# Kernel optimization log

Measured on AMD Instinct MI355X. Metric: run time of the kernel, lower is better.

The kernel has to match this reference:

```python
import jax, jax.numpy as jnp
import numpy as np

B, S, H, I, E, TOPK = 2, 2048, 1024, 2048, 8, 2


def setup_inputs() -> dict:
    key = jax.random.key(0)
    ks = jax.random.split(key, 6)
    return {
        "x": jax.random.normal(ks[0], (B, S, H), dtype=jnp.float32),
        "expert_indices": jax.random.randint(ks[1], (B, S, TOPK), 0, E, dtype=jnp.int64),
        "expert_weights": jax.random.uniform(ks[2], (B, S, TOPK), dtype=jnp.float32),
        "gate_proj": jax.random.normal(ks[3], (E, I, H), dtype=jnp.float32) * 0.02,
        "up_proj": jax.random.normal(ks[4], (E, I, H), dtype=jnp.float32) * 0.02,
        "down_proj": jax.random.normal(ks[5], (E, H, I), dtype=jnp.float32) * 0.02,
    }


def reference(x, expert_indices, expert_weights, gate_proj, up_proj, down_proj):
    # x: [B,S,H]; expert_indices/weights: [B,S,K]; gate/up: [E,I,H]; down: [E,H,I]
    b, s, h = x.shape
    e = gate_proj.shape[0]
    xf = x.reshape(-1, h)                      # [T,H]
    t = xf.shape[0]
    idx = expert_indices.reshape(t, -1)        # [T,K]
    w = expert_weights.reshape(t, -1)          # [T,K]
    # Combine per-(token,slot) weights into a per-(token,expert) weight matrix.
    # Identical math to the per-expert index_add_ in the torch module.
    we = jnp.zeros((t, e), dtype=x.dtype).at[jnp.arange(t)[:, None], idx].add(w)  # [T,E]
    gate = jax.nn.silu(jnp.einsum('th,eih->tei', xf, gate_proj))  # [T,E,I]
    up = jnp.einsum('th,eih->tei', xf, up_proj)                   # [T,E,I]
    out_e = jnp.einsum('tei,ehi->teh', gate * up, down_proj)      # [T,E,H]
    out = jnp.einsum('te,teh->th', we, out_e)                     # [T,H]
    return out.reshape(b, s, h)
```

## Files before the change

kernel.cpp:

```cpp
#include <hip/hip_runtime.h>


#define H_DIM 1024
#define I_DIM 2048
#define N_EXP 8
#define N_TOK 4096
#define N_ENT 8192
#define CAP   9216

typedef __attribute__((ext_vector_type(8))) short bhalf8;
typedef __attribute__((ext_vector_type(4))) float floatx4;

__device__ __forceinline__ unsigned short f2bf(float f) {
  unsigned int u = __float_as_uint(f);
  u += 0x7fffu + ((u >> 16) & 1u);
  return (unsigned short)(u >> 16);
}

__device__ __forceinline__ void ld16(const void* g, void* l) {
  __builtin_amdgcn_global_load_lds(
      (const __attribute__((address_space(1))) unsigned int*)g,
      (__attribute__((address_space(3))) unsigned int*)l, 16, 0, 0);
}

__global__ __launch_bounds__(256) void route_kernel(
    const int* __restrict__ idx, const float* __restrict__ wts,
    int* __restrict__ perm, float* __restrict__ pw, int* __restrict__ inv,
    int* __restrict__ counts, int* __restrict__ poff)
{
  __shared__ int cnt[N_EXP], cur[N_EXP], off[N_EXP];
  const int t = threadIdx.x;
  if (t < N_EXP) { cnt[t] = 0; cur[t] = 0; }
  __syncthreads();
  for (int i = t; i < N_ENT; i += 256) atomicAdd(&cnt[idx[i] & 7], 1);
  __syncthreads();
  if (t == 0) {
    int o = 0;
    for (int e = 0; e < N_EXP; e++) {
      off[e] = o; counts[e] = cnt[e]; poff[e] = o;
      o += ((cnt[e] + 127) >> 7) << 7;
    }
  }
  __syncthreads();
  for (int i = t; i < N_ENT; i += 256) {
    int e = idx[i] & 7;
    int p = atomicAdd(&cur[e], 1);
    int pos = off[e] + p;
    perm[pos] = i >> 1;
    pw[pos] = wts[i];
    inv[i] = pos;
  }
}

#define XE  4194304u
#define GE  20971520u
#define UE  37748736u
#define DE  54525952u
__global__ __launch_bounds__(256) void cast_all_kernel(
    const float* __restrict__ x, const float* __restrict__ g4,
    const float* __restrict__ u4, const float* __restrict__ d4,
    unsigned short* __restrict__ dst)
{
  unsigned int g = (blockIdx.x * 256u + threadIdx.x) * 8u;
  const float* s;
  if (g < XE)      s = x  + g;
  else if (g < GE) s = g4 + (g - XE);
  else if (g < UE) s = u4 + (g - GE);
  else             s = d4 + (g - UE);
  const float4* sp = (const float4*)s;
  float4 a = sp[0], b = sp[1];
  bhalf8 o;
  o[0] = (short)f2bf(a.x); o[1] = (short)f2bf(a.y); o[2] = (short)f2bf(a.z); o[3] = (short)f2bf(a.w);
  o[4] = (short)f2bf(b.x); o[5] = (short)f2bf(b.y); o[6] = (short)f2bf(b.z); o[7] = (short)f2bf(b.w);
  *(bhalf8*)(dst + g) = o;
}

__global__ __launch_bounds__(512, 4) void gemm1_kernel(
    const unsigned short* __restrict__ xb,
    const unsigned short* __restrict__ gbw,
    const unsigned short* __restrict__ ubw,
    const int* __restrict__ perm,
    const int* __restrict__ counts,
    const int* __restrict__ poff,
    unsigned short* __restrict__ act)
{
  const int e = blockIdx.z;
  const int Ne = counts[e];
  const int mt = blockIdx.y;
  if (mt * 256 >= Ne) return;
  const int NeR = ((Ne + 127) >> 7) << 7;
  const int base = poff[e];
  const int n0 = blockIdx.x * 64;

  __shared__ __align__(16) unsigned short As[256 * 64];
  __shared__ __align__(16) unsigned short Bgs[64 * 64];
  __shared__ __align__(16) unsigned short Bus[64 * 64];

  const int tid = threadIdx.x;
  const int lane = tid & 63;
  const int w = tid >> 6;
  const int wmi = w >> 1;
  const int wnj = w & 1;
  const int i3 = lane >> 3, i7 = lane & 7;
  const int swc = (i7 ^ i3) * 8;

  const unsigned short* pA[4]; unsigned short* lA[4];
#pragma unroll
  for (int t = 0; t < 4; t++) {
    int rloc = w * 32 + t * 8 + i3;
    int rr = mt * 256 + rloc; rr = rr < Ne ? rr : Ne - 1;
    pA[t] = xb + (size_t)perm[base + rr] * H_DIM + swc;
    lA[t] = &As[(w * 32 + t * 8) * 64];
  }
  const int nloc = w * 8 + i3;
  const size_t wb = (size_t)e * (I_DIM * H_DIM) + (size_t)(n0 + nloc) * H_DIM + swc;
  const unsigned short* pBg = gbw + wb;
  const unsigned short* pBu = ubw + wb;
  unsigned short* lBg = &Bgs[(w * 8) * 64];
  unsigned short* lBu = &Bus[(w * 8) * 64];

  floatx4 zero = {0.f, 0.f, 0.f, 0.f};
  floatx4 accg[4][2], accu[4][2];
#pragma unroll
  for (int i = 0; i < 4; i++)
#pragma unroll
    for (int j = 0; j < 2; j++) { accg[i][j] = zero; accu[i][j] = zero; }

  const int quad = lane >> 4, lm = lane & 15;
  const int s7 = lm & 7;

  for (int k0 = 0; k0 < H_DIM; k0 += 64) {
    __syncthreads();
#pragma unroll
    for (int t = 0; t < 4; t++) ld16(pA[t] + k0, lA[t]);
    ld16(pBg + k0, lBg);
    ld16(pBu + k0, lBu);
    __syncthreads();
#pragma unroll
    for (int kk = 0; kk < 2; kk++) {
      const int kq = kk * 4 + quad;
      const int ko = (kq ^ s7) * 8;
      bhalf8 a[4], bg[2], bu[2];
#pragma unroll
      for (int i = 0; i < 4; i++)
        a[i] = *(const bhalf8*)&As[(wmi * 64 + i * 16 + lm) * 64 + ko];
#pragma unroll
      for (int j = 0; j < 2; j++) {
        bg[j] = *(const bhalf8*)&Bgs[(wnj * 32 + j * 16 + lm) * 64 + ko];
        bu[j] = *(const bhalf8*)&Bus[(wnj * 32 + j * 16 + lm) * 64 + ko];
      }
#pragma unroll
      for (int i = 0; i < 4; i++)
#pragma unroll
        for (int j = 0; j < 2; j++) {
          accg[i][j] = __builtin_amdgcn_mfma_f32_16x16x32_bf16(a[i], bg[j], accg[i][j], 0, 0, 0);
          accu[i][j] = __builtin_amdgcn_mfma_f32_16x16x32_bf16(a[i], bu[j], accu[i][j], 0, 0, 0);
        }
    }
  }

#pragma unroll
  for (int i = 0; i < 4; i++) {
#pragma unroll
    for (int r = 0; r < 4; r++) {
      int row = mt * 256 + wmi * 64 + i * 16 + quad * 4 + r;
      if (row < NeR) {
        size_t rowoff = (size_t)(base + row) * I_DIM;
#pragma unroll
        for (int j = 0; j < 2; j++) {
          int col = n0 + wnj * 32 + j * 16 + lm;
          float g = accg[i][j][r];
          float u = accu[i][j][r];
          float h = (g / (1.f + __expf(-g))) * u;
          act[rowoff + col] = (unsigned short)f2bf(h);
        }
      }
    }
  }
}

__global__ __launch_bounds__(512, 4) void gemm2_kernel(
    const unsigned short* __restrict__ act,
    const unsigned short* __restrict__ dbw,
    const float* __restrict__ pw,
    const int* __restrict__ counts,
    const int* __restrict__ poff,
    float* __restrict__ ent)
{
  const int e = blockIdx.z;
  const int Ne = counts[e];
  const int mt = blockIdx.y;
  if (mt * 256 >= Ne) return;
  const int NeR = ((Ne + 127) >> 7) << 7;
  const int base = poff[e];
  const int n0 = (blockIdx.x & 7) * 128;
  const int k_lo = (blockIdx.x >> 3) * (I_DIM / 2);

  __shared__ __align__(16) unsigned short As[256 * 64];
  __shared__ __align__(16) unsigned short Bs[128 * 64];

  const int tid = threadIdx.x;
  const int lane = tid & 63;
  const int w = tid >> 6;
  const int wmi = w >> 1, wnj = w & 1;
  const int i3 = lane >> 3, i7 = lane & 7;
  const int swc = (i7 ^ i3) * 8;

  const unsigned short* pA[4]; unsigned short* lA[4];
#pragma unroll
  for (int t = 0; t < 4; t++) {
    int rloc = w * 32 + t * 8 + i3;
    int rr = mt * 256 + rloc; rr = rr < NeR ? rr : NeR - 1;
    pA[t] = act + (size_t)(base + rr) * I_DIM + k_lo + swc;
    lA[t] = &As[(w * 32 + t * 8) * 64];
  }
  const unsigned short* pB[2]; unsigned short* lB[2];
#pragma unroll
  for (int t = 0; t < 2; t++) {
    int rloc = w * 16 + t * 8 + i3;
    pB[t] = dbw + (size_t)e * (H_DIM * I_DIM) + (size_t)(n0 + rloc) * I_DIM + k_lo + swc;
    lB[t] = &Bs[(w * 16 + t * 8) * 64];
  }

  floatx4 zero = {0.f, 0.f, 0.f, 0.f};
  floatx4 acc[4][4];
#pragma unroll
  for (int i = 0; i < 4; i++)
#pragma unroll
    for (int j = 0; j < 4; j++) acc[i][j] = zero;

  const int quad = lane >> 4, lm = lane & 15;
  const int s7 = lm & 7;

  for (int k0 = 0; k0 < I_DIM / 2; k0 += 64) {
    __syncthreads();
#pragma unroll
    for (int t = 0; t < 4; t++) ld16(pA[t] + k0, lA[t]);
#pragma unroll
    for (int t = 0; t < 2; t++) ld16(pB[t] + k0, lB[t]);
    __syncthreads();
#pragma unroll
    for (int kk = 0; kk < 2; kk++) {
      const int kq = kk * 4 + quad;
      const int ko = (kq ^ s7) * 8;
      bhalf8 a[4], b[4];
#pragma unroll
      for (int i = 0; i < 4; i++)
        a[i] = *(const bhalf8*)&As[(wmi * 64 + i * 16 + lm) * 64 + ko];
#pragma unroll
      for (int j = 0; j < 4; j++)
        b[j] = *(const bhalf8*)&Bs[(wnj * 64 + j * 16 + lm) * 64 + ko];
#pragma unroll
      for (int i = 0; i < 4; i++)
#pragma unroll
        for (int j = 0; j < 4; j++)
          acc[i][j] = __builtin_amdgcn_mfma_f32_16x16x32_bf16(a[i], b[j], acc[i][j], 0, 0, 0);
    }
  }

  float* enth = ent + (size_t)(blockIdx.x >> 3) * CAP * H_DIM;
#pragma unroll
  for (int i = 0; i < 4; i++) {
#pragma unroll
    for (int r = 0; r < 4; r++) {
      int row = mt * 256 + wmi * 64 + i * 16 + quad * 4 + r;
      if (row < Ne) {
        float wt = pw[base + row];
        float* orow = enth + (size_t)(base + row) * H_DIM;
#pragma unroll
        for (int j = 0; j < 4; j++) {
          int col = n0 + wnj * 64 + j * 16 + lm;
          orow[col] = wt * acc[i][j][r];
        }
      }
    }
  }
}

__global__ __launch_bounds__(256) void combine_kernel(
    const float* __restrict__ ent, const int* __restrict__ inv,
    float* __restrict__ out)
{
  const int t = blockIdx.x;
  const int p0 = inv[2 * t], p1 = inv[2 * t + 1];
  const float4* r0 = (const float4*)(ent + (size_t)p0 * H_DIM);
  const float4* r1 = (const float4*)(ent + (size_t)p1 * H_DIM);
  const float4* r2 = (const float4*)(ent + (size_t)(CAP + p0) * H_DIM);
  const float4* r3 = (const float4*)(ent + (size_t)(CAP + p1) * H_DIM);
  float4 a = r0[threadIdx.x], b = r1[threadIdx.x];
  float4 c = r2[threadIdx.x], d = r3[threadIdx.x];
  float4 o = {a.x + b.x + c.x + d.x, a.y + b.y + c.y + d.y,
              a.z + b.z + c.z + d.z, a.w + b.w + c.w + d.w};
  ((float4*)(out + (size_t)t * H_DIM))[threadIdx.x] = o;
}

extern "C" void kernel_launch(void* const* d_in, const int* in_sizes, int n_in,
                              void* d_out, int out_size, void* d_ws, size_t ws_size,
                              hipStream_t stream) {
  const float* x    = (const float*)d_in[0];
  const int*   idx  = (const int*)d_in[1];
  const float* wts  = (const float*)d_in[2];
  const float* gate = (const float*)d_in[3];
  const float* up   = (const float*)d_in[4];
  const float* down = (const float*)d_in[5];
  float* out = (float*)d_out;
  char* ws = (char*)d_ws;

  unsigned short* bfs = (unsigned short*)(ws + 0);
  unsigned short* xb  = (unsigned short*)(ws + 0);
  unsigned short* gbw = (unsigned short*)(ws + 8388608);
  unsigned short* ubw = (unsigned short*)(ws + 41943040);
  unsigned short* dbw = (unsigned short*)(ws + 75497472);
  float*          ent = (float*)(ws + 0);
  unsigned short* act = (unsigned short*)(ws + 109051904);
  int*   perm   = (int*)(ws + 146800640);
  float* pw     = (float*)(ws + 146837504);
  int*   inv    = (int*)(ws + 146874368);
  int*   counts = (int*)(ws + 146907136);
  int*   poff   = (int*)(ws + 146907200);

  route_kernel<<<1, 256, 0, stream>>>(idx, wts, perm, pw, inv, counts, poff);

  cast_all_kernel<<<DE / 2048, 256, 0, stream>>>(x, gate, up, down, bfs);

  gemm1_kernel<<<dim3(I_DIM / 64, 32, N_EXP), 512, 0, stream>>>(
      xb, gbw, ubw, perm, counts, poff, act);

  gemm2_kernel<<<dim3(16, 32, N_EXP), 512, 0, stream>>>(
      act, dbw, pw, counts, poff, ent);

  combine_kernel<<<N_TOK, 256, 0, stream>>>(ent, inv, out);
}
```

Before: 427.4 us.

## Fuse fp32-to-bf16 weight conversion into GEMM B-tile loads

Drops the standalone pass that cast all three expert weight tensors to bf16. The GEMM kernels now read fp32 weights directly into registers, pack them to bf16 with a perm-based round, and store them to LDS in a k-major layout. The next tile is prefetched into registers so the load overlaps the MFMA work. This removes a large read-write pass over the weights, but weight tiles are reloaded as fp32 (twice the bytes) by every M-tile block. Rounding also changes from round-to-nearest-even to round-half-up.

Measured after the change: 416.3 us. -2.6%, faster.

```diff
diff --git a/kernel.cpp b/kernel.cpp
--- a/kernel.cpp
+++ b/kernel.cpp
@@ -15,6 +15,12 @@
   unsigned int u = __float_as_uint(f);
   u += 0x7fffu + ((u >> 16) & 1u);
   return (unsigned short)(u >> 16);
+}
+
+__device__ __forceinline__ unsigned int pkbf(float a, float b) {
+  unsigned int ua = __float_as_uint(a) + 0x8000u;
+  unsigned int ub = __float_as_uint(b) + 0x8000u;
+  return __builtin_amdgcn_perm(ub, ua, 0x07060302u);
 }
 
 __device__ __forceinline__ void ld16(const void* g, void* l) {
@@ -52,33 +58,22 @@
   }
 }
 
-#define XE  4194304u
-#define GE  20971520u
-#define UE  37748736u
-#define DE  54525952u
-__global__ __launch_bounds__(256) void cast_all_kernel(
-    const float* __restrict__ x, const float* __restrict__ g4,
-    const float* __restrict__ u4, const float* __restrict__ d4,
-    unsigned short* __restrict__ dst)
-{
-  unsigned int g = (blockIdx.x * 256u + threadIdx.x) * 8u;
-  const float* s;
-  if (g < XE)      s = x  + g;
-  else if (g < GE) s = g4 + (g - XE);
-  else if (g < UE) s = u4 + (g - GE);
-  else             s = d4 + (g - UE);
-  const float4* sp = (const float4*)s;
+__global__ __launch_bounds__(256) void cast_x_kernel(
+    const float* __restrict__ s, unsigned short* __restrict__ d)
+{
+  int i = (blockIdx.x * 256 + threadIdx.x) * 8;
+  const float4* sp = (const float4*)(s + i);
   float4 a = sp[0], b = sp[1];
   bhalf8 o;
   o[0] = (short)f2bf(a.x); o[1] = (short)f2bf(a.y); o[2] = (short)f2bf(a.z); o[3] = (short)f2bf(a.w);
   o[4] = (short)f2bf(b.x); o[5] = (short)f2bf(b.y); o[6] = (short)f2bf(b.z); o[7] = (short)f2bf(b.w);
-  *(bhalf8*)(dst + g) = o;
+  *(bhalf8*)(d + i) = o;
 }
 
 __global__ __launch_bounds__(512, 4) void gemm1_kernel(
     const unsigned short* __restrict__ xb,
-    const unsigned short* __restrict__ gbw,
-    const unsigned short* __restrict__ ubw,
+    const float* __restrict__ gw,
+    const float* __restrict__ uw,
     const int* __restrict__ perm,
     const int* __restrict__ counts,
     const int* __restrict__ poff,
@@ -112,12 +107,12 @@
     pA[t] = xb + (size_t)perm[base + rr] * H_DIM + swc;
     lA[t] = &As[(w * 32 + t * 8) * 64];
   }
-  const int nloc = w * 8 + i3;
-  const size_t wb = (size_t)e * (I_DIM * H_DIM) + (size_t)(n0 + nloc) * H_DIM + swc;
-  const unsigned short* pBg = gbw + wb;
-  const unsigned short* pBu = ubw + wb;
-  unsigned short* lBg = &Bgs[(w * 8) * 64];
-  unsigned short* lBu = &Bus[(w * 8) * 64];
+  const int nlocB = w * 8 + i3;
+  const size_t wb = (size_t)e * (I_DIM * H_DIM) + (size_t)(n0 + nlocB) * H_DIM + i7 * 8;
+  const float* pg = gw + wb;
+  const float* pu = uw + wb;
+  unsigned short* lBg = &Bgs[(i7 * 64 + nlocB) * 8];
+  unsigned short* lBu = &Bus[(i7 * 64 + nlocB) * 8];
 
   floatx4 zero = {0.f, 0.f, 0.f, 0.f};
   floatx4 accg[4][2], accu[4][2];
@@ -129,13 +124,26 @@
   const int quad = lane >> 4, lm = lane & 15;
   const int s7 = lm & 7;
 
+  float4 g0 = *(const float4*)(pg);
+  float4 g1 = *(const float4*)(pg + 4);
+  float4 u0 = *(const float4*)(pu);
+  float4 u1 = *(const float4*)(pu + 4);
+
   for (int k0 = 0; k0 < H_DIM; k0 += 64) {
     __syncthreads();
 #pragma unroll
     for (int t = 0; t < 4; t++) ld16(pA[t] + k0, lA[t]);
-    ld16(pBg + k0, lBg);
-    ld16(pBu + k0, lBu);
+    *(uint4*)lBg = make_uint4(pkbf(g0.x, g0.y), pkbf(g0.z, g0.w),
+                              pkbf(g1.x, g1.y), pkbf(g1.z, g1.w));
+    *(uint4*)lBu = make_uint4(pkbf(u0.x, u0.y), pkbf(u0.z, u0.w),
+                              pkbf(u1.x, u1.y), pkbf(u1.z, u1.w));
     __syncthreads();
+    if (k0 + 64 < H_DIM) {
+      g0 = *(const float4*)(pg + k0 + 64);
+      g1 = *(const float4*)(pg + k0 + 68);
+      u0 = *(const float4*)(pu + k0 + 64);
+      u1 = *(const float4*)(pu + k0 + 68);
+    }
 #pragma unroll
     for (int kk = 0; kk < 2; kk++) {
       const int kq = kk * 4 + quad;
@@ -146,8 +154,8 @@
         a[i] = *(const bhalf8*)&As[(wmi * 64 + i * 16 + lm) * 64 + ko];
 #pragma unroll
       for (int j = 0; j < 2; j++) {
-        bg[j] = *(const bhalf8*)&Bgs[(wnj * 32 + j * 16 + lm) * 64 + ko];
-        bu[j] = *(const bhalf8*)&Bus[(wnj * 32 + j * 16 + lm) * 64 + ko];
+        bg[j] = *(const bhalf8*)&Bgs[(kq * 64 + wnj * 32 + j * 16 + lm) * 8];
+        bu[j] = *(const bhalf8*)&Bus[(kq * 64 + wnj * 32 + j * 16 + lm) * 8];
       }
 #pragma unroll
       for (int i = 0; i < 4; i++)
@@ -181,7 +189,7 @@
 
 __global__ __launch_bounds__(512, 4) void gemm2_kernel(
     const unsigned short* __restrict__ act,
-    const unsigned short* __restrict__ dbw,
+    const float* __restrict__ dw,
     const float* __restrict__ pw,
     const int* __restrict__ counts,
     const int* __restrict__ poff,
@@ -214,12 +222,12 @@
     pA[t] = act + (size_t)(base + rr) * I_DIM + k_lo + swc;
     lA[t] = &As[(w * 32 + t * 8) * 64];
   }
-  const unsigned short* pB[2]; unsigned short* lB[2];
+  const float* pB[2]; unsigned short* lB[2];
 #pragma unroll
   for (int t = 0; t < 2; t++) {
     int rloc = w * 16 + t * 8 + i3;
-    pB[t] = dbw + (size_t)e * (H_DIM * I_DIM) + (size_t)(n0 + rloc) * I_DIM + k_lo + swc;
-    lB[t] = &Bs[(w * 16 + t * 8) * 64];
+    pB[t] = dw + (size_t)e * (H_DIM * I_DIM) + (size_t)(n0 + rloc) * I_DIM + k_lo + i7 * 8;
+    lB[t] = &Bs[(i7 * 128 + rloc) * 8];
   }
 
   floatx4 zero = {0.f, 0.f, 0.f, 0.f};
@@ -232,13 +240,26 @@
   const int quad = lane >> 4, lm = lane & 15;
   const int s7 = lm & 7;
 
+  float4 b00 = *(const float4*)(pB[0]);
+  float4 b01 = *(const float4*)(pB[0] + 4);
+  float4 b10 = *(const float4*)(pB[1]);
+  float4 b11 = *(const float4*)(pB[1] + 4);
+
   for (int k0 = 0; k0 < I_DIM / 2; k0 += 64) {
     __syncthreads();
 #pragma unroll
     for (int t = 0; t < 4; t++) ld16(pA[t] + k0, lA[t]);
-#pragma unroll
-    for (int t = 0; t < 2; t++) ld16(pB[t] + k0, lB[t]);
+    *(uint4*)lB[0] = make_uint4(pkbf(b00.x, b00.y), pkbf(b00.z, b00.w),
+                                pkbf(b01.x, b01.y), pkbf(b01.z, b01.w));
+    *(uint4*)lB[1] = make_uint4(pkbf(b10.x, b10.y), pkbf(b10.z, b10.w),
+                                pkbf(b11.x, b11.y), pkbf(b11.z, b11.w));
     __syncthreads();
+    if (k0 + 64 < I_DIM / 2) {
+      b00 = *(const float4*)(pB[0] + k0 + 64);
+      b01 = *(const float4*)(pB[0] + k0 + 68);
+      b10 = *(const float4*)(pB[1] + k0 + 64);
+      b11 = *(const float4*)(pB[1] + k0 + 68);
+    }
 #pragma unroll
     for (int kk = 0; kk < 2; kk++) {
       const int kq = kk * 4 + quad;
@@ -249,7 +270,7 @@
         a[i] = *(const bhalf8*)&As[(wmi * 64 + i * 16 + lm) * 64 + ko];
 #pragma unroll
       for (int j = 0; j < 4; j++)
-        b[j] = *(const bhalf8*)&Bs[(wnj * 64 + j * 16 + lm) * 64 + ko];
+        b[j] = *(const bhalf8*)&Bs[(kq * 128 + wnj * 64 + j * 16 + lm) * 8];
 #pragma unroll
       for (int i = 0; i < 4; i++)
 #pragma unroll
@@ -306,28 +327,24 @@
   float* out = (float*)d_out;
   char* ws = (char*)d_ws;
 
-  unsigned short* bfs = (unsigned short*)(ws + 0);
-  unsigned short* xb  = (unsigned short*)(ws + 0);
-  unsigned short* gbw = (unsigned short*)(ws + 8388608);
-  unsigned short* ubw = (unsigned short*)(ws + 41943040);
-  unsigned short* dbw = (unsigned short*)(ws + 75497472);
   float*          ent = (float*)(ws + 0);
-  unsigned short* act = (unsigned short*)(ws + 109051904);
-  int*   perm   = (int*)(ws + 146800640);
-  float* pw     = (float*)(ws + 146837504);
-  int*   inv    = (int*)(ws + 146874368);
-  int*   counts = (int*)(ws + 146907136);
-  int*   poff   = (int*)(ws + 146907200);
+  unsigned short* act = (unsigned short*)(ws + 75497472);
+  unsigned short* xb  = (unsigned short*)(ws + 113246208);
+  int*   perm   = (int*)(ws + 121634816);
+  float* pw     = (float*)(ws + 121671680);
+  int*   inv    = (int*)(ws + 121708544);
+  int*   counts = (int*)(ws + 121741312);
+  int*   poff   = (int*)(ws + 121741376);
 
   route_kernel<<<1, 256, 0, stream>>>(idx, wts, perm, pw, inv, counts, poff);
 
-  cast_all_kernel<<<DE / 2048, 256, 0, stream>>>(x, gate, up, down, bfs);
+  cast_x_kernel<<<(N_TOK * H_DIM) / (256 * 8), 256, 0, stream>>>(x, xb);
 
   gemm1_kernel<<<dim3(I_DIM / 64, 32, N_EXP), 512, 0, stream>>>(
-      xb, gbw, ubw, perm, counts, poff, act);
+      xb, gate, up, perm, counts, poff, act);
 
   gemm2_kernel<<<dim3(16, 32, N_EXP), 512, 0, stream>>>(
-      act, dbw, pw, counts, poff, ent);
+      act, down, pw, counts, poff, ent);
 
   combine_kernel<<<N_TOK, 256, 0, stream>>>(ent, inv, out);
 }
```
